# Kernel tuning notes

Measured on AMD Instinct MI355X. Metric: run time of the kernel, lower is better.

## Reference

```python
import jax, jax.numpy as jnp
import numpy as np

B, D, H, C, V, SAMPLE_NUM = 4096, 1024, 512, 50, 4, 10000


def ds_combin_two(alpha1, alpha2, K):
    """Dempster-Shafer combination of two Dirichlet parameter sets [B, K]."""
    S1 = jnp.sum(alpha1, axis=1, keepdims=True)
    S2 = jnp.sum(alpha2, axis=1, keepdims=True)
    b1 = (alpha1 - 1.0) / S1
    b2 = (alpha2 - 1.0) / S2
    u1 = K / S1  # [B,1]
    u2 = K / S2
    # bb_sum - bb_diag computed without materializing [B,K,K] outer product:
    # sum_ij b1_i b2_j = sum(b1)*sum(b2); diag sum = sum_i b1_i b2_i
    Cconf = jnp.sum(b1, axis=1) * jnp.sum(b2, axis=1) - jnp.sum(b1 * b2, axis=1)  # [B]
    denom = (1.0 - Cconf)[:, None]
    b_a = (b1 * b2 + b1 * u2 + b2 * u1) / denom
    u_a = (u1 * u2) / denom  # [B,1]
    S_a = K / u_a
    e_a = b_a * S_a
    return e_a + 1.0


def setup_inputs() -> dict:
    key = jax.random.key(0)
    ks = jax.random.split(key, 8)
    x = jax.random.normal(ks[0], (V, B, D), dtype=jnp.float32)
    indexes = jax.random.randint(ks[1], (B,), 0, SAMPLE_NUM)
    W1 = jax.random.normal(ks[2], (V, D, H), dtype=jnp.float32) * (1.0 / np.sqrt(D))
    b1 = jax.random.normal(ks[3], (V, H), dtype=jnp.float32) * 0.01
    W2 = jax.random.normal(ks[4], (V, H, C), dtype=jnp.float32) * (1.0 / np.sqrt(H))
    b2 = jax.random.normal(ks[5], (V, C), dtype=jnp.float32) * 0.01
    # original init: identity per (view, sample); add small noise so the
    eye = jnp.eye(C, dtype=jnp.float32)
    matrixes = eye[None, None] + 0.01 * jax.random.normal(ks[6], (V, SAMPLE_NUM, C, C), dtype=jnp.float32)
    return {"x": x, "indexes": indexes, "W1": W1, "b1": b1, "W2": W2, "b2": b2, "matrixes": matrixes}


def reference(x, indexes, W1, b1, W2, b2, matrixes):
    K = W2.shape[-1]
    n_views = x.shape[0]
    # per-view classifier MLP: Linear->ReLU->Linear->Softplus
    h = jax.nn.relu(jnp.einsum("vbd,vdh->vbh", x, W1) + b1[:, None, :])
    evidence = jax.nn.softplus(jnp.einsum("vbh,vhc->vbc", h, W2) + b2[:, None, :])  # [V,B,C]
    # transferByMatrix (training path): per-sample gathered [C,C] matmul
    sel = matrixes[:, indexes]  # [V,B,C,C]
    transferred = jnp.einsum("vbc,vbcd->vbd", evidence, sel)  # [V,B,C]
    t_alpha = transferred + 1.0
    # sequential DS combination over views
    alpha_a = t_alpha[0]
    for v in range(1, n_views):
        alpha_a = ds_combin_two(alpha_a, t_alpha[v], K)
    evidence_a = alpha_a - 1.0  # [B,C]
    return transferred, evidence_a, evidence
```

## Files before the change

### kernel.cpp

```cpp
#include <hip/hip_runtime.h>
#include <math.h>

typedef unsigned short u16;
typedef __attribute__((ext_vector_type(8))) short bf16x8;
typedef __attribute__((ext_vector_type(4))) float f32x4;

#define DEVI __device__ __forceinline__

constexpr int NV = 4;
constexpr int NB = 4096;
constexpr int ND = 1024;
constexpr int NH = 512;
constexpr int NC = 50;
constexpr int NSAMP = 10000;
constexpr int NCP = 64;

DEVI u16 to_bf16(float f) {
  union { float f; unsigned u; } v; v.f = f;
  unsigned r = v.u + 0x7fffu + ((v.u >> 16) & 1u);
  return (u16)(r >> 16);
}

DEVI float wsum(float x) {
#pragma unroll
  for (int m = 32; m > 0; m >>= 1) x += __shfl_xor(x, m, 64);
  return x;
}

#define GLD_LDS16(gsrc, ldst)                                                  \
  __builtin_amdgcn_global_load_lds(                                            \
      (const __attribute__((address_space(1))) void*)(gsrc),                   \
      (__attribute__((address_space(3))) void*)(ldst), 16, 0, 0)

__global__ __launch_bounds__(256) void k_convert_x(const float* __restrict__ x,
                                                   u16* __restrict__ xb) {
  const long n4 = (long)NV * NB * ND / 4;
  long i = (long)blockIdx.x * blockDim.x + threadIdx.x;
  const long stride = (long)gridDim.x * blockDim.x;
  for (; i < n4; i += stride) {
    float4 f = ((const float4*)x)[i];
    ushort4 o;
    o.x = to_bf16(f.x); o.y = to_bf16(f.y);
    o.z = to_bf16(f.z); o.w = to_bf16(f.w);
    ((ushort4*)xb)[i] = o;
  }
}

__global__ __launch_bounds__(256) void k_transpose_w1(const float* __restrict__ W1,
                                                      u16* __restrict__ W1T) {
  __shared__ float tile[32][33];
  const int v = blockIdx.z;
  const int d0 = blockIdx.x * 32;
  const int h0 = blockIdx.y * 32;
  const float* src = W1 + (size_t)v * ND * NH;
  u16* dst = W1T + (size_t)v * NH * ND;
  const int tx = threadIdx.x, ty = threadIdx.y;
#pragma unroll
  for (int j = 0; j < 32; j += 8)
    tile[ty + j][tx] = src[(size_t)(d0 + ty + j) * NH + h0 + tx];
  __syncthreads();
#pragma unroll
  for (int j = 0; j < 32; j += 8)
    dst[(size_t)(h0 + ty + j) * ND + d0 + tx] = to_bf16(tile[tx][ty + j]);
}

__global__ __launch_bounds__(256) void k_prep_w2(const float* __restrict__ W2,
                                                 u16* __restrict__ W2T) {
  int i = blockIdx.x * blockDim.x + threadIdx.x;
  if (i >= NV * NCP * NH) return;
  int h = i % NH;
  int c = (i / NH) % NCP;
  int v = i / (NCP * NH);
  float val = (c < NC) ? W2[((size_t)v * NH + h) * NC + c] : 0.f;
  W2T[i] = to_bf16(val);
}

__global__ __launch_bounds__(256) void k_gemm1(const u16* __restrict__ Xb,
                                               const u16* __restrict__ W1T,
                                               const float* __restrict__ b1,
                                               u16* __restrict__ Hb) {
  constexpr int BM = 128, BN = 128, BK = 32;
  const int v = blockIdx.z;
  const int m0 = blockIdx.x * BM;
  const int n0 = blockIdx.y * BN;
  __shared__ u16 As[BM][BK];
  __shared__ u16 Bs[BN][BK];
  const u16* Ag = Xb + (size_t)v * NB * ND + (size_t)m0 * ND;
  const u16* Bg = W1T + (size_t)v * NH * ND + (size_t)n0 * ND;
  const int tid = threadIdx.x;
  const int lane = tid & 63;
  const int wv = tid >> 6;
  const int wr = wv >> 1, wc = wv & 1;
  const int r = tid >> 2;
  const int c8 = (tid & 3) * 8;

  f32x4 acc[4][4] = {};

  for (int k0 = 0; k0 < ND; k0 += BK) {
    __syncthreads();
    GLD_LDS16(Ag + (size_t)r * ND + k0 + c8,        &As[r][c8]);
    GLD_LDS16(Ag + (size_t)(r + 64) * ND + k0 + c8, &As[r + 64][c8]);
    GLD_LDS16(Bg + (size_t)r * ND + k0 + c8,        &Bs[r][c8]);
    GLD_LDS16(Bg + (size_t)(r + 64) * ND + k0 + c8, &Bs[r + 64][c8]);
    __syncthreads();

    const int fr = lane & 15;
    const int kb = (lane >> 4) * 8;
    bf16x8 af[4], bf[4];
#pragma unroll
    for (int mi = 0; mi < 4; ++mi)
      af[mi] = *(const bf16x8*)&As[wr * 64 + mi * 16 + fr][kb];
#pragma unroll
    for (int ni = 0; ni < 4; ++ni)
      bf[ni] = *(const bf16x8*)&Bs[wc * 64 + ni * 16 + fr][kb];
#pragma unroll
    for (int mi = 0; mi < 4; ++mi)
#pragma unroll
      for (int ni = 0; ni < 4; ++ni)
        acc[mi][ni] = __builtin_amdgcn_mfma_f32_16x16x32_bf16(
            af[mi], bf[ni], acc[mi][ni], 0, 0, 0);
  }

  const int frow = (lane >> 4) * 4;
  const int fcol = lane & 15;
#pragma unroll
  for (int mi = 0; mi < 4; ++mi) {
#pragma unroll
    for (int ni = 0; ni < 4; ++ni) {
      const int n = n0 + wc * 64 + ni * 16 + fcol;
      const float bias = b1[v * NH + n];
#pragma unroll
      for (int j = 0; j < 4; ++j) {
        const int m = m0 + wr * 64 + mi * 16 + frow + j;
        float val = fmaxf(acc[mi][ni][j] + bias, 0.f);
        Hb[(size_t)v * NB * NH + (size_t)m * NH + n] = to_bf16(val);
      }
    }
  }
}

__global__ __launch_bounds__(256) void k_gemm2(const u16* __restrict__ Hb,
                                               const u16* __restrict__ W2T,
                                               const float* __restrict__ b2,
                                               float* __restrict__ out_ev) {
  constexpr int BM = 64, BK = 32;
  const int v = blockIdx.z;
  const int m0 = blockIdx.x * BM;
  __shared__ u16 As[BM][BK];
  __shared__ u16 Bs[NCP][BK];
  const u16* Ag = Hb + (size_t)v * NB * NH + (size_t)m0 * NH;
  const u16* Bg = W2T + (size_t)v * NCP * NH;
  const int tid = threadIdx.x;
  const int lane = tid & 63;
  const int wv = tid >> 6;
  const int r = tid >> 2;
  const int c8 = (tid & 3) * 8;

  f32x4 acc[4] = {};

  for (int k0 = 0; k0 < NH; k0 += BK) {
    __syncthreads();
    GLD_LDS16(Ag + (size_t)r * NH + k0 + c8, &As[r][c8]);
    GLD_LDS16(Bg + (size_t)r * NH + k0 + c8, &Bs[r][c8]);
    __syncthreads();

    const int fr = lane & 15;
    const int kb = (lane >> 4) * 8;
    bf16x8 af = *(const bf16x8*)&As[wv * 16 + fr][kb];
#pragma unroll
    for (int ni = 0; ni < 4; ++ni) {
      bf16x8 bf = *(const bf16x8*)&Bs[ni * 16 + fr][kb];
      acc[ni] = __builtin_amdgcn_mfma_f32_16x16x32_bf16(af, bf, acc[ni], 0, 0, 0);
    }
  }

  const int frow = (lane >> 4) * 4;
  const int fcol = lane & 15;
#pragma unroll
  for (int ni = 0; ni < 4; ++ni) {
    const int n = ni * 16 + fcol;
    if (n < NC) {
      const float bias = b2[v * NC + n];
#pragma unroll
      for (int j = 0; j < 4; ++j) {
        const int m = m0 + wv * 16 + frow + j;
        float x = acc[ni][j] + bias;
        float sp = fmaxf(x, 0.f) + log1pf(expf(-fabsf(x)));
        out_ev[(size_t)v * NB * NC + (size_t)m * NC + n] = sp;
      }
    }
  }
}

__global__ __launch_bounds__(256) void k_transfer(const float* __restrict__ evf,
                                                  const float* __restrict__ mats,
                                                  const int* __restrict__ idx,
                                                  float* __restrict__ out_tr) {
  const int gw = blockIdx.x * 4 + (threadIdx.x >> 6);
  const int lane = threadIdx.x & 63;
  if (gw >= NV * NB) return;
  const int v = gw >> 12;
  const int b = gw & (NB - 1);
  const float* e = evf + ((size_t)v * NB + b) * NC;
  const float* M = mats + ((size_t)v * NSAMP + idx[b]) * NC * NC;
  if (lane < NC) {
    float acc = 0.f;
#pragma unroll
    for (int c = 0; c < NC; ++c)
      acc = fmaf(e[c], M[c * NC + lane], acc);
    out_tr[((size_t)v * NB + b) * NC + lane] = acc;
  }
}

__global__ __launch_bounds__(256) void k_combine(const float* __restrict__ trf,
                                                 float* __restrict__ out_ea) {
  const int b = blockIdx.x * 4 + (threadIdx.x >> 6);
  const int lane = threadIdx.x & 63;
  if (b >= NB) return;
  const bool act = lane < NC;
  const float Kf = (float)NC;

  float ta[NV];
#pragma unroll
  for (int v = 0; v < NV; ++v)
    ta[v] = act ? trf[((size_t)v * NB + b) * NC + lane] + 1.0f : 0.0f;

  float alpha = ta[0];
#pragma unroll
  for (int v = 1; v < NV; ++v) {
    float a2 = ta[v];
    float S1 = wsum(act ? alpha : 0.f);
    float S2 = wsum(act ? a2 : 0.f);
    float b1v = act ? (alpha - 1.f) / S1 : 0.f;
    float b2v = act ? (a2 - 1.f) / S2 : 0.f;
    float u1 = Kf / S1, u2 = Kf / S2;
    float sb1 = wsum(b1v);
    float sb2 = wsum(b2v);
    float sb12 = wsum(b1v * b2v);
    float Cconf = sb1 * sb2 - sb12;
    float denom = 1.f - Cconf;
    float b_a = (b1v * b2v + b1v * u2 + b2v * u1) / denom;
    float u_a = u1 * u2 / denom;
    float S_a = Kf / u_a;
    alpha = b_a * S_a + 1.f;
  }
  if (act) out_ea[(size_t)b * NC + lane] = alpha - 1.f;
}

extern "C" void kernel_launch(void* const* d_in, const int* in_sizes, int n_in,
                              void* d_out, int out_size, void* d_ws, size_t ws_size,
                              hipStream_t stream) {
  const float *x = nullptr, *W1 = nullptr, *b1 = nullptr, *W2 = nullptr,
              *b2 = nullptr, *mats = nullptr;
  const int* idx = nullptr;
  for (int i = 0; i < n_in; ++i) {
    switch (in_sizes[i]) {
      case 16777216:  x    = (const float*)d_in[i]; break;
      case 4096:      idx  = (const int*)d_in[i];   break;
      case 2097152:   W1   = (const float*)d_in[i]; break;
      case 2048:      b1   = (const float*)d_in[i]; break;
      case 102400:    W2   = (const float*)d_in[i]; break;
      case 200:       b2   = (const float*)d_in[i]; break;
      case 100000000: mats = (const float*)d_in[i]; break;
      default: break;
    }
  }
  if (!x || !idx || !W1 || !b1 || !W2 || !b2 || !mats) return;

  char* ws = (char*)d_ws;
  u16* xb  = (u16*)(ws + 0);
  u16* w1t = (u16*)(ws + 33554432);
  u16* w2t = (u16*)(ws + 37748736);
  u16* hb  = (u16*)(ws + 38010880);

  float* out_tr = (float*)d_out;
  float* out_ea = out_tr + (size_t)NV * NB * NC;
  float* out_ev = out_ea + (size_t)NB * NC;

  k_convert_x<<<4096, 256, 0, stream>>>(x, xb);
  k_transpose_w1<<<dim3(ND / 32, NH / 32, NV), dim3(32, 8), 0, stream>>>(W1, w1t);
  k_prep_w2<<<(NV * NCP * NH + 255) / 256, 256, 0, stream>>>(W2, w2t);
  k_gemm1<<<dim3(NB / 128, NH / 128, NV), 256, 0, stream>>>(xb, w1t, b1, hb);
  k_gemm2<<<dim3(NB / 64, 1, NV), 256, 0, stream>>>(hb, w2t, b2, out_ev);
  k_transfer<<<NV * NB / 4, 256, 0, stream>>>(out_ev, mats, idx, out_tr);
  k_combine<<<NB / 4, 256, 0, stream>>>(out_tr, out_ea);
}
```

Before: 102.8 us.

## Fuse bf16 conversion of x into gemm1 and merge transfer with combine

Removes the standalone fp32-to-bf16 conversion pass over x by converting in registers inside gemm1's A-tile load, saving the bf16 workspace write and one launch. Also fuses the per-sample transfer matmul into the DS combine kernel so transferred values need not be re-read. In exchange gemm1 reads fp32 A (twice the bytes, once per column tile) with synchronous register loads instead of async LDS loads, and the fused tail kernel has a quarter as many waves, each processing views serially.

```diff
diff --git a/kernel.cpp b/kernel.cpp
--- a/kernel.cpp
+++ b/kernel.cpp
@@ -31,20 +31,6 @@
   __builtin_amdgcn_global_load_lds(                                            \
       (const __attribute__((address_space(1))) void*)(gsrc),                   \
       (__attribute__((address_space(3))) void*)(ldst), 16, 0, 0)
-
-__global__ __launch_bounds__(256) void k_convert_x(const float* __restrict__ x,
-                                                   u16* __restrict__ xb) {
-  const long n4 = (long)NV * NB * ND / 4;
-  long i = (long)blockIdx.x * blockDim.x + threadIdx.x;
-  const long stride = (long)gridDim.x * blockDim.x;
-  for (; i < n4; i += stride) {
-    float4 f = ((const float4*)x)[i];
-    ushort4 o;
-    o.x = to_bf16(f.x); o.y = to_bf16(f.y);
-    o.z = to_bf16(f.z); o.w = to_bf16(f.w);
-    ((ushort4*)xb)[i] = o;
-  }
-}
 
 __global__ __launch_bounds__(256) void k_transpose_w1(const float* __restrict__ W1,
                                                       u16* __restrict__ W1T) {
@@ -75,7 +61,7 @@
   W2T[i] = to_bf16(val);
 }
 
-__global__ __launch_bounds__(256) void k_gemm1(const u16* __restrict__ Xb,
+__global__ __launch_bounds__(256) void k_gemm1(const float* __restrict__ Xf,
                                                const u16* __restrict__ W1T,
                                                const float* __restrict__ b1,
                                                u16* __restrict__ Hb) {
@@ -85,23 +71,39 @@
   const int n0 = blockIdx.y * BN;
   __shared__ u16 As[BM][BK];
   __shared__ u16 Bs[BN][BK];
-  const u16* Ag = Xb + (size_t)v * NB * ND + (size_t)m0 * ND;
+  const float* Ag = Xf + (size_t)v * NB * ND + (size_t)m0 * ND;
   const u16* Bg = W1T + (size_t)v * NH * ND + (size_t)n0 * ND;
   const int tid = threadIdx.x;
   const int lane = tid & 63;
   const int wv = tid >> 6;
   const int wr = wv >> 1, wc = wv & 1;
-  const int r = tid >> 2;
-  const int c8 = (tid & 3) * 8;
+  const int rB = tid >> 2;
+  const int cB = (tid & 3) * 8;
+  const int rA = tid >> 1;
+  const int cA = (tid & 1) * 16;
 
   f32x4 acc[4][4] = {};
 
   for (int k0 = 0; k0 < ND; k0 += BK) {
     __syncthreads();
-    GLD_LDS16(Ag + (size_t)r * ND + k0 + c8,        &As[r][c8]);
-    GLD_LDS16(Ag + (size_t)(r + 64) * ND + k0 + c8, &As[r + 64][c8]);
-    GLD_LDS16(Bg + (size_t)r * ND + k0 + c8,        &Bs[r][c8]);
-    GLD_LDS16(Bg + (size_t)(r + 64) * ND + k0 + c8, &Bs[r + 64][c8]);
+    GLD_LDS16(Bg + (size_t)rB * ND + k0 + cB,        &Bs[rB][cB]);
+    GLD_LDS16(Bg + (size_t)(rB + 64) * ND + k0 + cB, &Bs[rB + 64][cB]);
+    {
+      const float* ap = Ag + (size_t)rA * ND + k0 + cA;
+      float4 f0 = ((const float4*)ap)[0];
+      float4 f1 = ((const float4*)ap)[1];
+      float4 f2 = ((const float4*)ap)[2];
+      float4 f3 = ((const float4*)ap)[3];
+      ushort4 u0, u1, u2, u3;
+      u0.x = to_bf16(f0.x); u0.y = to_bf16(f0.y); u0.z = to_bf16(f0.z); u0.w = to_bf16(f0.w);
+      u1.x = to_bf16(f1.x); u1.y = to_bf16(f1.y); u1.z = to_bf16(f1.z); u1.w = to_bf16(f1.w);
+      u2.x = to_bf16(f2.x); u2.y = to_bf16(f2.y); u2.z = to_bf16(f2.z); u2.w = to_bf16(f2.w);
+      u3.x = to_bf16(f3.x); u3.y = to_bf16(f3.y); u3.z = to_bf16(f3.z); u3.w = to_bf16(f3.w);
+      *(ushort4*)&As[rA][cA]     = u0;
+      *(ushort4*)&As[rA][cA + 4] = u1;
+      *(ushort4*)&As[rA][cA + 8] = u2;
+      *(ushort4*)&As[rA][cA + 12]= u3;
+    }
     __syncthreads();
 
     const int fr = lane & 15;
@@ -192,38 +194,32 @@
   }
 }
 
-__global__ __launch_bounds__(256) void k_transfer(const float* __restrict__ evf,
-                                                  const float* __restrict__ mats,
-                                                  const int* __restrict__ idx,
-                                                  float* __restrict__ out_tr) {
-  const int gw = blockIdx.x * 4 + (threadIdx.x >> 6);
-  const int lane = threadIdx.x & 63;
-  if (gw >= NV * NB) return;
-  const int v = gw >> 12;
-  const int b = gw & (NB - 1);
-  const float* e = evf + ((size_t)v * NB + b) * NC;
-  const float* M = mats + ((size_t)v * NSAMP + idx[b]) * NC * NC;
-  if (lane < NC) {
-    float acc = 0.f;
-#pragma unroll
-    for (int c = 0; c < NC; ++c)
-      acc = fmaf(e[c], M[c * NC + lane], acc);
-    out_tr[((size_t)v * NB + b) * NC + lane] = acc;
-  }
-}
-
-__global__ __launch_bounds__(256) void k_combine(const float* __restrict__ trf,
-                                                 float* __restrict__ out_ea) {
+__global__ __launch_bounds__(256) void k_tc(const float* __restrict__ evf,
+                                            const float* __restrict__ mats,
+                                            const int* __restrict__ idx,
+                                            float* __restrict__ out_tr,
+                                            float* __restrict__ out_ea) {
   const int b = blockIdx.x * 4 + (threadIdx.x >> 6);
   const int lane = threadIdx.x & 63;
   if (b >= NB) return;
   const bool act = lane < NC;
   const float Kf = (float)NC;
+  const int ix = idx[b];
 
   float ta[NV];
 #pragma unroll
-  for (int v = 0; v < NV; ++v)
-    ta[v] = act ? trf[((size_t)v * NB + b) * NC + lane] + 1.0f : 0.0f;
+  for (int v = 0; v < NV; ++v) {
+    float acc = 0.f;
+    if (act) {
+      const float* e = evf + ((size_t)v * NB + b) * NC;
+      const float* M = mats + ((size_t)v * NSAMP + ix) * NC * NC;
+#pragma unroll
+      for (int c = 0; c < NC; ++c)
+        acc = fmaf(e[c], M[c * NC + lane], acc);
+      out_tr[((size_t)v * NB + b) * NC + lane] = acc;
+    }
+    ta[v] = act ? acc + 1.0f : 0.0f;
+  }
 
   float alpha = ta[0];
 #pragma unroll
@@ -268,20 +264,17 @@
   if (!x || !idx || !W1 || !b1 || !W2 || !b2 || !mats) return;
 
   char* ws = (char*)d_ws;
-  u16* xb  = (u16*)(ws + 0);
-  u16* w1t = (u16*)(ws + 33554432);
-  u16* w2t = (u16*)(ws + 37748736);
-  u16* hb  = (u16*)(ws + 38010880);
+  u16* w1t = (u16*)(ws + 0);
+  u16* w2t = (u16*)(ws + 4194304);
+  u16* hb  = (u16*)(ws + 4456448);
 
   float* out_tr = (float*)d_out;
   float* out_ea = out_tr + (size_t)NV * NB * NC;
   float* out_ev = out_ea + (size_t)NB * NC;
 
-  k_convert_x<<<4096, 256, 0, stream>>>(x, xb);
   k_transpose_w1<<<dim3(ND / 32, NH / 32, NV), dim3(32, 8), 0, stream>>>(W1, w1t);
   k_prep_w2<<<(NV * NCP * NH + 255) / 256, 256, 0, stream>>>(W2, w2t);
-  k_gemm1<<<dim3(NB / 128, NH / 128, NV), 256, 0, stream>>>(xb, w1t, b1, hb);
+  k_gemm1<<<dim3(NB / 128, NH / 128, NV), 256, 0, stream>>>(x, w1t, b1, hb);
   k_gemm2<<<dim3(NB / 64, 1, NV), 256, 0, stream>>>(hb, w2t, b2, out_ev);
-  k_transfer<<<NV * NB / 4, 256, 0, stream>>>(out_ev, mats, idx, out_tr);
-  k_combine<<<NB / 4, 256, 0, stream>>>(out_tr, out_ea);
-}
+  k_tc<<<NB / 4, 256, 0, stream>>>(out_ev, mats, idx, out_tr, out_ea);
+}
```

After: 99.22 us. 1.04x faster.
